# Kernel optimization log

Measured on AMD Instinct MI355X. Metric: run time of the kernel, lower is better.

The kernel has to match this reference:

```python
import jax, jax.numpy as jnp
import numpy as np

IMG_H, IMG_W = 16, 16
N = IMG_H * IMG_W              # 256 tokens
HEADS = 8
HEAD_DIM = 32
INNER = HEADS * HEAD_DIM       # 256
IN_CH = 256
OUT_CH = 256
BATCH = 64
SCALE = HEAD_DIM ** -0.5


def _make_relative_index():
    # Mirrors the torch buffer construction exactly.
    coords = np.stack(np.meshgrid(np.arange(IMG_H), np.arange(IMG_W), indexing='ij'))
    coords = coords.reshape(2, -1)                      # (2, N)
    rel = coords[:, :, None] - coords[:, None, :]       # (2, N, N)
    rel[0] += IMG_H - 1
    rel[1] += IMG_W - 1
    rel[0] *= 2 * IMG_W - 1
    idx = rel.sum(0).reshape(-1)                        # (N*N,) values in [0, (2H-1)(2W-1))
    return idx.astype(np.int32)


def setup_inputs() -> dict:
    key = jax.random.key(0)
    k1, k2, k3, k4, k5 = jax.random.split(key, 5)
    x = jax.random.normal(k1, (BATCH, N, IN_CH), dtype=jnp.float32)
    w_qkv = jax.random.normal(k2, (IN_CH, 3 * INNER), dtype=jnp.float32) * 0.02
    bias_table = jax.random.normal(k3, ((2 * IMG_H - 1) * (2 * IMG_W - 1), HEADS), dtype=jnp.float32) * 0.02
    w_out = jax.random.normal(k4, (INNER, OUT_CH), dtype=jnp.float32) * 0.02
    b_out = jax.random.normal(k5, (OUT_CH,), dtype=jnp.float32) * 0.02
    rel_index = jnp.asarray(_make_relative_index())
    return {"x": x, "w_qkv": w_qkv, "bias_table": bias_table,
            "w_out": w_out, "b_out": b_out, "rel_index": rel_index}


def reference(x, w_qkv, bias_table, w_out, b_out, rel_index):
    b, n, _ = x.shape
    qkv = x @ w_qkv                                     # (b, n, 3*inner)
    q, k, v = jnp.split(qkv, 3, axis=-1)
    def heads(t):
        return t.reshape(b, n, HEADS, HEAD_DIM).transpose(0, 2, 1, 3)  # (b, h, n, d)
    q, k, v = heads(q), heads(k), heads(v)
    dots = jnp.einsum('bhid,bhjd->bhij', q, k) * SCALE  # (b, h, n, n)
    # gather relative position bias: (n*n, h) -> (1, h, n, n)
    rel_bias = bias_table[rel_index].reshape(n, n, HEADS).transpose(2, 0, 1)[None]
    attn = jax.nn.softmax(dots + rel_bias, axis=-1)
    out = jnp.einsum('bhij,bhjd->bhid', attn, v)        # (b, h, n, d)
    out = out.transpose(0, 2, 1, 3).reshape(b, n, INNER)
    return out @ w_out + b_out
```

## Files before the change

kernel.cpp:

```cpp
#include <hip/hip_runtime.h>
#include <hip/hip_bf16.h>

typedef __bf16 bfv8 __attribute__((ext_vector_type(8)));
typedef float f32x4 __attribute__((ext_vector_type(4)));
typedef unsigned short u16;
typedef unsigned int u32;
typedef u16 u16x8 __attribute__((ext_vector_type(8)));

__device__ __forceinline__ float bf2f(u16 u){ union{u32 i; float f;} x; x.i=(u32)u<<16; return x.f; }
__device__ __forceinline__ u16 f2bf(float f){ union{float f; u32 i;} x; x.f=f; u32 i=x.i; return (u16)((i + 0x7FFFu + ((i>>16)&1u))>>16); }

__global__ __launch_bounds__(256) void transpose_k(const float* __restrict__ in, u16* __restrict__ out, int R, int C){
  __shared__ u16 tile[32][34];
  int c0 = blockIdx.x*32, r0 = blockIdx.y*32;
  int tx = threadIdx.x & 31, ty = threadIdx.x >> 5;
  #pragma unroll
  for(int dy=0; dy<32; dy+=8) tile[ty+dy][tx] = f2bf(in[(size_t)(r0+ty+dy)*C + (c0+tx)]);
  __syncthreads();
  #pragma unroll
  for(int dy=0; dy<32; dy+=8) out[(size_t)(c0+ty+dy)*R + (r0+tx)] = tile[tx][ty+dy];
}

__global__ __launch_bounds__(256) void biasgather_k(const float* __restrict__ bt, const int* __restrict__ ridx, u16* __restrict__ biasp2){
  const float L2E = 1.4426950408889634f;
  int idx = blockIdx.x*256 + threadIdx.x;
  int e = idx & 7, ch = (idx>>3)&7, lane = (idx>>6)&63, rb = (idx>>12)&15, h = (idx>>16)&7;
  int ll = lane & 15, lg = lane >> 4;
  int tj = ch*2 + (e>>2), r = e & 3;
  int q = rb*16 + ll, k = 16*tj + 4*lg + r;
  biasp2[idx] = f2bf(bt[ridx[q*256 + k]*8 + h] * L2E);
}

template<bool BIAS, typename OUT, bool AF32, int TM>
__global__ __launch_bounds__(256,4) void gemm_k(const void* __restrict__ Av, const u16* __restrict__ Bt,
                         const float* __restrict__ bias, OUT* __restrict__ C, int M, int N, int K){
  constexpr int MI = TM/32;
  __shared__ u16 As[TM][40];
  __shared__ u16 Bs[128][40];
  const int tid = threadIdx.x, lane = tid & 63, wv = tid >> 6;
  const int lg = lane >> 4, ll = lane & 15;
  const int wr = (wv >> 1)*(TM/2), wc = (wv & 1)*64;
  const size_t m0 = (size_t)blockIdx.x*TM;
  const int n0 = blockIdx.y*128;
  f32x4 acc[MI][4] = {};
  for(int k0=0; k0<K; k0+=32){
    #pragma unroll
    for(int p=0;p<TM/64;++p){
      int ch = tid + p*256;
      int row = ch >> 2, c8 = (ch & 3)*8;
      if constexpr (AF32){
        const float* Af = (const float*)Av;
        float4 a = *(const float4*)&Af[(m0+row)*(size_t)K + k0 + c8];
        float4 b = *(const float4*)&Af[(m0+row)*(size_t)K + k0 + c8 + 4];
        u16 r[8] = { f2bf(a.x),f2bf(a.y),f2bf(a.z),f2bf(a.w), f2bf(b.x),f2bf(b.y),f2bf(b.z),f2bf(b.w) };
        *(int4*)&As[row][c8] = *(int4*)r;
      } else {
        const u16* Ab = (const u16*)Av;
        *(int4*)&As[row][c8] = *(const int4*)&Ab[(m0+row)*(size_t)K + k0 + c8];
      }
    }
    #pragma unroll
    for(int p=0;p<2;++p){
      int ch = tid + p*256;
      int row = ch >> 2, c8 = (ch & 3)*8;
      *(int4*)&Bs[row][c8] = *(const int4*)&Bt[(size_t)(n0+row)*K + k0 + c8];
    }
    __syncthreads();
    bfv8 af[MI], bfr[4];
    #pragma unroll
    for(int i=0;i<MI;++i) af[i] = *(const bfv8*)&As[wr+16*i+ll][lg*8];
    #pragma unroll
    for(int j=0;j<4;++j) bfr[j] = *(const bfv8*)&Bs[wc+16*j+ll][lg*8];
    #pragma unroll
    for(int i=0;i<MI;++i)
      #pragma unroll
      for(int j=0;j<4;++j)
        acc[i][j] = __builtin_amdgcn_mfma_f32_16x16x32_bf16(af[i], bfr[j], acc[i][j], 0,0,0);
    __syncthreads();
  }
  #pragma unroll
  for(int i=0;i<MI;++i)
    #pragma unroll
    for(int j=0;j<4;++j){
      int col = n0 + wc + 16*j + ll;
      float bv = 0.f;
      if (BIAS) bv = bias[col];
      #pragma unroll
      for(int r=0;r<4;++r){
        size_t row = m0 + wr + 16*i + lg*4 + r;
        float v = acc[i][j][r] + bv;
        if constexpr (sizeof(OUT) == 2) C[row*(size_t)N + col] = f2bf(v);
        else                            C[row*(size_t)N + col] = v;
      }
    }
}

__global__ __launch_bounds__(256,3) void attn_k(const u16* __restrict__ qkv, const u16* __restrict__ biasp2, u16* __restrict__ attnb){
  __shared__ u16 Ks[256*40];
  __shared__ u16 Vt[32*264];
  const int bh = blockIdx.x >> 2, quarter = blockIdx.x & 3;
  const int b = bh >> 3, h = bh & 7;
  const int tid = threadIdx.x, lane = tid & 63, wv = tid >> 6;
  const int lg = lane >> 4, ll = lane & 15;
  const u16* qb = qkv + (size_t)b*256*768;
  const int q0 = quarter*64 + wv*16;
  const u16* bp = biasp2 + ((((size_t)h*16 + (q0>>4))*64 + lane) << 6);
  u16x8 bias[8];
  #pragma unroll
  for(int g=0; g<8; ++g) bias[g] = *(const u16x8*)&bp[g*8];
  bfv8 qf = *(const bfv8*)&qb[(size_t)(q0+ll)*768 + h*32 + lg*8];
  #pragma unroll
  for(int p=0;p<4;++p){
    int ch = tid + p*256;
    int j = ch >> 2, d8 = (ch & 3)*8;
    *(int4*)&Ks[j*40 + d8] = *(const int4*)&qb[(size_t)j*768 + 256 + h*32 + d8];
  }
  #pragma unroll
  for(int it=0; it<16; ++it){
    int e = tid + it*256;
    int j = e >> 4, dp = (e & 15)*2;
    int jp = ((j>>5)<<5) + 8*((j>>2)&3) + 4*((j>>4)&1) + (j&3);
    u32 v = *(const u32*)&qb[(size_t)j*768 + 512 + h*32 + dp];
    Vt[dp*264 + jp]     = (u16)(v & 0xffffu);
    Vt[(dp+1)*264 + jp] = (u16)(v >> 16);
  }
  __syncthreads();
  f32x4 s[16];
  const f32x4 zero = {0.f,0.f,0.f,0.f};
  #pragma unroll
  for(int tj=0;tj<16;++tj){
    bfv8 kf = *(const bfv8*)&Ks[(16*tj+ll)*40 + lg*8];
    s[tj] = __builtin_amdgcn_mfma_f32_16x16x32_bf16(kf, qf, zero, 0,0,0);
  }
  const float SCALE2 = 0.17677669529663687f * 1.4426950408889634f;
  f32x4 sm = {0.f,0.f,0.f,0.f};
  #pragma unroll
  for(int tj=0;tj<16;++tj){
    #pragma unroll
    for(int r=0;r<4;++r){
      float p = exp2f(fmaf(s[tj][r], SCALE2, bf2f(bias[tj>>1][4*(tj&1)+r])));
      s[tj][r] = p;
      sm[r] += p;
    }
  }
  float sum = sm[0]+sm[1]+sm[2]+sm[3];
  sum += __shfl_xor(sum,16);
  sum += __shfl_xor(sum,32);
  float rinv = 1.0f/sum;
  u32 pk[16][2];
  #pragma unroll
  for(int tj=0;tj<16;++tj){
    asm("v_cvt_pk_bf16_f32 %0, %1, %2" : "=v"(pk[tj][0]) : "v"(s[tj][0]), "v"(s[tj][1]));
    asm("v_cvt_pk_bf16_f32 %0, %1, %2" : "=v"(pk[tj][1]) : "v"(s[tj][2]), "v"(s[tj][3]));
  }
  f32x4 o[2] = {zero, zero};
  #pragma unroll
  for(int c=0;c<8;++c){
    union { u32 u[4]; bfv8 v; } pu;
    pu.u[0] = pk[2*c][0]; pu.u[1] = pk[2*c][1]; pu.u[2] = pk[2*c+1][0]; pu.u[3] = pk[2*c+1][1];
    bfv8 pf = pu.v;
    #pragma unroll
    for(int td=0;td<2;++td){
      bfv8 vf = *(const bfv8*)&Vt[(16*td+ll)*264 + 32*c + lg*8];
      o[td] = __builtin_amdgcn_mfma_f32_16x16x32_bf16(pf, vf, o[td], 0,0,0);
    }
  }
  #pragma unroll
  for(int td=0;td<2;++td)
    #pragma unroll
    for(int r=0;r<4;++r){
      float rl = __shfl(rinv, 4*lg + r);
      int row = q0 + 4*lg + r;
      attnb[((size_t)b*256 + row)*256 + h*32 + 16*td + ll] = f2bf(o[td][r]*rl);
    }
}

extern "C" void kernel_launch(void* const* d_in, const int* in_sizes, int n_in,
                              void* d_out, int out_size, void* d_ws, size_t ws_size,
                              hipStream_t stream) {
  const float* x     = (const float*)d_in[0];
  const float* w_qkv = (const float*)d_in[1];
  const float* btab  = (const float*)d_in[2];
  const float* w_out = (const float*)d_in[3];
  const float* b_out = (const float*)d_in[4];
  const int*   ridx  = (const int*)d_in[5];
  float* out = (float*)d_out;

  char* ws = (char*)d_ws;
  size_t off = 0;
  u16*   wT     = (u16*)(ws + off); off += (size_t)768*256*2;
  u16*   woT    = (u16*)(ws + off); off += (size_t)256*256*2;
  u16*   biasp2 = (u16*)(ws + off); off += (size_t)524288*2;
  u16*   qkvb   = (u16*)(ws + off); off += (size_t)64*256*768*2;
  u16*   attnb  = (u16*)(ws + off); off += (size_t)64*256*256*2;

  transpose_k<<<dim3(24,8),256,0,stream>>>(w_qkv, wT, 256, 768);
  transpose_k<<<dim3(8,8),256,0,stream>>>(w_out, woT, 256, 256);
  biasgather_k<<<2048,256,0,stream>>>(btab, ridx, biasp2);
  gemm_k<false,u16,true,128><<<dim3(128,6),256,0,stream>>>(x, wT, nullptr, qkvb, 16384, 768, 256);
  attn_k<<<2048,256,0,stream>>>(qkvb, biasp2, attnb);
  gemm_k<true,float,false,64><<<dim3(256,2),256,0,stream>>>(attnb, woT, b_out, out, 16384, 256, 256);
}
```

Measured before the change: 66.56 us.

## Merge prep kernels, pre-convert x, use direct LDS loads, loop attention quarters

Folds the two weight transposes and the bias gather into one prep kernel, which also converts x to bf16 up front. The GEMM now stages A and B tiles with global_load_lds straight into LDS using a K-step of 64. The attention kernel loads K/V once per (batch, head) and loops over the four query quarters instead of launching four blocks that each reload them. This cuts launch count and redundant K/V staging. The costs are an extra pass that writes and rereads a bf16 copy of x, a smaller attention grid (512 blocks), and unpadded LDS rows in the GEMM that may cause bank conflicts.

```diff
diff --git a/kernel.cpp b/kernel.cpp
--- a/kernel.cpp
+++ b/kernel.cpp
@@ -10,72 +10,94 @@
 __device__ __forceinline__ float bf2f(u16 u){ union{u32 i; float f;} x; x.i=(u32)u<<16; return x.f; }
 __device__ __forceinline__ u16 f2bf(float f){ union{float f; u32 i;} x; x.f=f; u32 i=x.i; return (u16)((i + 0x7FFFu + ((i>>16)&1u))>>16); }
 
-__global__ __launch_bounds__(256) void transpose_k(const float* __restrict__ in, u16* __restrict__ out, int R, int C){
+__device__ __forceinline__ void gl16(const void* g, void* l){
+  __builtin_amdgcn_global_load_lds((const __attribute__((address_space(1))) unsigned int*)g,
+                                   (__attribute__((address_space(3))) unsigned int*)l, 16, 0, 0);
+}
+
+__global__ __launch_bounds__(256) void prep_k(const float* __restrict__ x, u16* __restrict__ xb,
+                                              const float* __restrict__ w_qkv, u16* __restrict__ wT,
+                                              const float* __restrict__ w_out, u16* __restrict__ woT,
+                                              const float* __restrict__ bt, const int* __restrict__ ridx,
+                                              u16* __restrict__ biasp2){
   __shared__ u16 tile[32][34];
-  int c0 = blockIdx.x*32, r0 = blockIdx.y*32;
-  int tx = threadIdx.x & 31, ty = threadIdx.x >> 5;
-  #pragma unroll
-  for(int dy=0; dy<32; dy+=8) tile[ty+dy][tx] = f2bf(in[(size_t)(r0+ty+dy)*C + (c0+tx)]);
-  __syncthreads();
-  #pragma unroll
-  for(int dy=0; dy<32; dy+=8) out[(size_t)(c0+ty+dy)*R + (r0+tx)] = tile[tx][ty+dy];
-}
-
-__global__ __launch_bounds__(256) void biasgather_k(const float* __restrict__ bt, const int* __restrict__ ridx, u16* __restrict__ biasp2){
-  const float L2E = 1.4426950408889634f;
-  int idx = blockIdx.x*256 + threadIdx.x;
-  int e = idx & 7, ch = (idx>>3)&7, lane = (idx>>6)&63, rb = (idx>>12)&15, h = (idx>>16)&7;
-  int ll = lane & 15, lg = lane >> 4;
-  int tj = ch*2 + (e>>2), r = e & 3;
-  int q = rb*16 + ll, k = 16*tj + 4*lg + r;
-  biasp2[idx] = f2bf(bt[ridx[q*256 + k]*8 + h] * L2E);
-}
-
-template<bool BIAS, typename OUT, bool AF32, int TM>
-__global__ __launch_bounds__(256,4) void gemm_k(const void* __restrict__ Av, const u16* __restrict__ Bt,
+  const int bid = blockIdx.x, tid = threadIdx.x;
+  if (bid < 2048){
+    int i = (bid*256 + tid)*8;
+    float4 a = *(const float4*)&x[i];
+    float4 b = *(const float4*)&x[i+4];
+    u16 r[8] = { f2bf(a.x),f2bf(a.y),f2bf(a.z),f2bf(a.w), f2bf(b.x),f2bf(b.y),f2bf(b.z),f2bf(b.w) };
+    *(int4*)&xb[i] = *(int4*)r;
+  } else if (bid < 2048+192){
+    int b2 = bid - 2048;
+    int c0 = (b2 % 24)*32, r0 = (b2/24)*32;
+    int tx = tid & 31, ty = tid >> 5;
+    #pragma unroll
+    for(int dy=0; dy<32; dy+=8) tile[ty+dy][tx] = f2bf(w_qkv[(size_t)(r0+ty+dy)*768 + (c0+tx)]);
+    __syncthreads();
+    #pragma unroll
+    for(int dy=0; dy<32; dy+=8) wT[(size_t)(c0+ty+dy)*256 + (r0+tx)] = tile[tx][ty+dy];
+  } else if (bid < 2048+192+64){
+    int b3 = bid - (2048+192);
+    int c0 = (b3 & 7)*32, r0 = (b3 >> 3)*32;
+    int tx = tid & 31, ty = tid >> 5;
+    #pragma unroll
+    for(int dy=0; dy<32; dy+=8) tile[ty+dy][tx] = f2bf(w_out[(size_t)(r0+ty+dy)*256 + (c0+tx)]);
+    __syncthreads();
+    #pragma unroll
+    for(int dy=0; dy<32; dy+=8) woT[(size_t)(c0+ty+dy)*256 + (r0+tx)] = tile[tx][ty+dy];
+  } else {
+    const float L2E = 1.4426950408889634f;
+    int idx = (bid - (2048+192+64))*256 + tid;
+    int e = idx & 7, ch = (idx>>3)&7, lane = (idx>>6)&63, rb = (idx>>12)&15, h = (idx>>16)&7;
+    int ll = lane & 15, lg = lane >> 4;
+    int tj = ch*2 + (e>>2), r = e & 3;
+    int q = rb*16 + ll, k = 16*tj + 4*lg + r;
+    biasp2[idx] = f2bf(bt[ridx[q*256 + k]*8 + h] * L2E);
+  }
+}
+
+template<bool BIAS, typename OUT, int TM>
+__global__ __launch_bounds__(256) void gemm_k(const u16* __restrict__ A, const u16* __restrict__ Bt,
                          const float* __restrict__ bias, OUT* __restrict__ C, int M, int N, int K){
   constexpr int MI = TM/32;
-  __shared__ u16 As[TM][40];
-  __shared__ u16 Bs[128][40];
+  __shared__ u16 As[TM*64];
+  __shared__ u16 Bs[128*64];
   const int tid = threadIdx.x, lane = tid & 63, wv = tid >> 6;
   const int lg = lane >> 4, ll = lane & 15;
   const int wr = (wv >> 1)*(TM/2), wc = (wv & 1)*64;
   const size_t m0 = (size_t)blockIdx.x*TM;
   const int n0 = blockIdx.y*128;
+  const int lrow = lane >> 3, lcol = (lane & 7)*8;
   f32x4 acc[MI][4] = {};
-  for(int k0=0; k0<K; k0+=32){
-    #pragma unroll
-    for(int p=0;p<TM/64;++p){
-      int ch = tid + p*256;
-      int row = ch >> 2, c8 = (ch & 3)*8;
-      if constexpr (AF32){
-        const float* Af = (const float*)Av;
-        float4 a = *(const float4*)&Af[(m0+row)*(size_t)K + k0 + c8];
-        float4 b = *(const float4*)&Af[(m0+row)*(size_t)K + k0 + c8 + 4];
-        u16 r[8] = { f2bf(a.x),f2bf(a.y),f2bf(a.z),f2bf(a.w), f2bf(b.x),f2bf(b.y),f2bf(b.z),f2bf(b.w) };
-        *(int4*)&As[row][c8] = *(int4*)r;
-      } else {
-        const u16* Ab = (const u16*)Av;
-        *(int4*)&As[row][c8] = *(const int4*)&Ab[(m0+row)*(size_t)K + k0 + c8];
-      }
-    }
-    #pragma unroll
-    for(int p=0;p<2;++p){
-      int ch = tid + p*256;
-      int row = ch >> 2, c8 = (ch & 3)*8;
-      *(int4*)&Bs[row][c8] = *(const int4*)&Bt[(size_t)(n0+row)*K + k0 + c8];
-    }
-    __syncthreads();
-    bfv8 af[MI], bfr[4];
-    #pragma unroll
-    for(int i=0;i<MI;++i) af[i] = *(const bfv8*)&As[wr+16*i+ll][lg*8];
-    #pragma unroll
-    for(int j=0;j<4;++j) bfr[j] = *(const bfv8*)&Bs[wc+16*j+ll][lg*8];
+  for(int k0=0; k0<K; k0+=64){
+    #pragma unroll
+    for(int c=0;c<MI;++c){
+      int rowbase = (wv*MI + c)*8;
+      gl16(&A[(m0 + rowbase + lrow)*(size_t)K + k0 + lcol], &As[rowbase*64]);
+    }
+    #pragma unroll
+    for(int c=0;c<4;++c){
+      int rowbase = (wv*4 + c)*8;
+      gl16(&Bt[(size_t)(n0 + rowbase + lrow)*K + k0 + lcol], &Bs[rowbase*64]);
+    }
+    __syncthreads();
+    bfv8 af[MI][2], bf[4][2];
     #pragma unroll
     for(int i=0;i<MI;++i)
       #pragma unroll
-      for(int j=0;j<4;++j)
-        acc[i][j] = __builtin_amdgcn_mfma_f32_16x16x32_bf16(af[i], bfr[j], acc[i][j], 0,0,0);
+      for(int kh=0;kh<2;++kh) af[i][kh] = *(const bfv8*)&As[(wr+16*i+ll)*64 + kh*32 + lg*8];
+    #pragma unroll
+    for(int j=0;j<4;++j)
+      #pragma unroll
+      for(int kh=0;kh<2;++kh) bf[j][kh] = *(const bfv8*)&Bs[(wc+16*j+ll)*64 + kh*32 + lg*8];
+    #pragma unroll
+    for(int kh=0;kh<2;++kh)
+      #pragma unroll
+      for(int i=0;i<MI;++i)
+        #pragma unroll
+        for(int j=0;j<4;++j)
+          acc[i][j] = __builtin_amdgcn_mfma_f32_16x16x32_bf16(af[i][kh], bf[j][kh], acc[i][j], 0,0,0);
     __syncthreads();
   }
   #pragma unroll
@@ -98,17 +120,10 @@
 __global__ __launch_bounds__(256,3) void attn_k(const u16* __restrict__ qkv, const u16* __restrict__ biasp2, u16* __restrict__ attnb){
   __shared__ u16 Ks[256*40];
   __shared__ u16 Vt[32*264];
-  const int bh = blockIdx.x >> 2, quarter = blockIdx.x & 3;
-  const int b = bh >> 3, h = bh & 7;
+  const int b = blockIdx.x >> 3, h = blockIdx.x & 7;
   const int tid = threadIdx.x, lane = tid & 63, wv = tid >> 6;
   const int lg = lane >> 4, ll = lane & 15;
   const u16* qb = qkv + (size_t)b*256*768;
-  const int q0 = quarter*64 + wv*16;
-  const u16* bp = biasp2 + ((((size_t)h*16 + (q0>>4))*64 + lane) << 6);
-  u16x8 bias[8];
-  #pragma unroll
-  for(int g=0; g<8; ++g) bias[g] = *(const u16x8*)&bp[g*8];
-  bfv8 qf = *(const bfv8*)&qb[(size_t)(q0+ll)*768 + h*32 + lg*8];
   #pragma unroll
   for(int p=0;p<4;++p){
     int ch = tid + p*256;
@@ -125,54 +140,63 @@
     Vt[(dp+1)*264 + jp] = (u16)(v >> 16);
   }
   __syncthreads();
-  f32x4 s[16];
+  const float SCALE2 = 0.17677669529663687f * 1.4426950408889634f;
   const f32x4 zero = {0.f,0.f,0.f,0.f};
-  #pragma unroll
-  for(int tj=0;tj<16;++tj){
-    bfv8 kf = *(const bfv8*)&Ks[(16*tj+ll)*40 + lg*8];
-    s[tj] = __builtin_amdgcn_mfma_f32_16x16x32_bf16(kf, qf, zero, 0,0,0);
-  }
-  const float SCALE2 = 0.17677669529663687f * 1.4426950408889634f;
-  f32x4 sm = {0.f,0.f,0.f,0.f};
-  #pragma unroll
-  for(int tj=0;tj<16;++tj){
-    #pragma unroll
-    for(int r=0;r<4;++r){
-      float p = exp2f(fmaf(s[tj][r], SCALE2, bf2f(bias[tj>>1][4*(tj&1)+r])));
-      s[tj][r] = p;
-      sm[r] += p;
-    }
-  }
-  float sum = sm[0]+sm[1]+sm[2]+sm[3];
-  sum += __shfl_xor(sum,16);
-  sum += __shfl_xor(sum,32);
-  float rinv = 1.0f/sum;
-  u32 pk[16][2];
-  #pragma unroll
-  for(int tj=0;tj<16;++tj){
-    asm("v_cvt_pk_bf16_f32 %0, %1, %2" : "=v"(pk[tj][0]) : "v"(s[tj][0]), "v"(s[tj][1]));
-    asm("v_cvt_pk_bf16_f32 %0, %1, %2" : "=v"(pk[tj][1]) : "v"(s[tj][2]), "v"(s[tj][3]));
-  }
-  f32x4 o[2] = {zero, zero};
-  #pragma unroll
-  for(int c=0;c<8;++c){
-    union { u32 u[4]; bfv8 v; } pu;
-    pu.u[0] = pk[2*c][0]; pu.u[1] = pk[2*c][1]; pu.u[2] = pk[2*c+1][0]; pu.u[3] = pk[2*c+1][1];
-    bfv8 pf = pu.v;
-    #pragma unroll
-    for(int td=0;td<2;++td){
-      bfv8 vf = *(const bfv8*)&Vt[(16*td+ll)*264 + 32*c + lg*8];
-      o[td] = __builtin_amdgcn_mfma_f32_16x16x32_bf16(pf, vf, o[td], 0,0,0);
-    }
-  }
-  #pragma unroll
-  for(int td=0;td<2;++td)
-    #pragma unroll
-    for(int r=0;r<4;++r){
-      float rl = __shfl(rinv, 4*lg + r);
-      int row = q0 + 4*lg + r;
-      attnb[((size_t)b*256 + row)*256 + h*32 + 16*td + ll] = f2bf(o[td][r]*rl);
-    }
+  #pragma unroll 1
+  for(int quarter=0; quarter<4; ++quarter){
+    const int q0 = quarter*64 + wv*16;
+    const u16* bp = biasp2 + ((((size_t)h*16 + (q0>>4))*64 + lane) << 6);
+    u16x8 bias[8];
+    #pragma unroll
+    for(int g=0; g<8; ++g) bias[g] = *(const u16x8*)&bp[g*8];
+    bfv8 qf = *(const bfv8*)&qb[(size_t)(q0+ll)*768 + h*32 + lg*8];
+    f32x4 s[16];
+    #pragma unroll
+    for(int tj=0;tj<16;++tj){
+      bfv8 kf = *(const bfv8*)&Ks[(16*tj+ll)*40 + lg*8];
+      s[tj] = __builtin_amdgcn_mfma_f32_16x16x32_bf16(kf, qf, zero, 0,0,0);
+    }
+    f32x4 sm = {0.f,0.f,0.f,0.f};
+    #pragma unroll
+    for(int tj=0;tj<16;++tj){
+      #pragma unroll
+      for(int r=0;r<4;++r){
+        float p = exp2f(fmaf(s[tj][r], SCALE2, bf2f(bias[tj>>1][4*(tj&1)+r])));
+        s[tj][r] = p;
+        sm[r] += p;
+      }
+    }
+    float sum = sm[0]+sm[1]+sm[2]+sm[3];
+    sum += __shfl_xor(sum,16);
+    sum += __shfl_xor(sum,32);
+    float rinv = 1.0f/sum;
+    u32 pk[16][2];
+    #pragma unroll
+    for(int tj=0;tj<16;++tj){
+      asm("v_cvt_pk_bf16_f32 %0, %1, %2" : "=v"(pk[tj][0]) : "v"(s[tj][0]), "v"(s[tj][1]));
+      asm("v_cvt_pk_bf16_f32 %0, %1, %2" : "=v"(pk[tj][1]) : "v"(s[tj][2]), "v"(s[tj][3]));
+    }
+    f32x4 o[2] = {zero, zero};
+    #pragma unroll
+    for(int c=0;c<8;++c){
+      union { u32 u[4]; bfv8 v; } pu;
+      pu.u[0] = pk[2*c][0]; pu.u[1] = pk[2*c][1]; pu.u[2] = pk[2*c+1][0]; pu.u[3] = pk[2*c+1][1];
+      bfv8 pf = pu.v;
+      #pragma unroll
+      for(int td=0;td<2;++td){
+        bfv8 vf = *(const bfv8*)&Vt[(16*td+ll)*264 + 32*c + lg*8];
+        o[td] = __builtin_amdgcn_mfma_f32_16x16x32_bf16(pf, vf, o[td], 0,0,0);
+      }
+    }
+    #pragma unroll
+    for(int td=0;td<2;++td)
+      #pragma unroll
+      for(int r=0;r<4;++r){
+        float rl = __shfl(rinv, 4*lg + r);
+        int row = q0 + 4*lg + r;
+        attnb[((size_t)b*256 + row)*256 + h*32 + 16*td + ll] = f2bf(o[td][r]*rl);
+      }
+  }
 }
 
 extern "C" void kernel_launch(void* const* d_in, const int* in_sizes, int n_in,
@@ -188,16 +212,15 @@
 
   char* ws = (char*)d_ws;
   size_t off = 0;
+  u16*   xb     = (u16*)(ws + off); off += (size_t)64*256*256*2;
   u16*   wT     = (u16*)(ws + off); off += (size_t)768*256*2;
   u16*   woT    = (u16*)(ws + off); off += (size_t)256*256*2;
   u16*   biasp2 = (u16*)(ws + off); off += (size_t)524288*2;
   u16*   qkvb   = (u16*)(ws + off); off += (size_t)64*256*768*2;
   u16*   attnb  = (u16*)(ws + off); off += (size_t)64*256*256*2;
 
-  transpose_k<<<dim3(24,8),256,0,stream>>>(w_qkv, wT, 256, 768);
-  transpose_k<<<dim3(8,8),256,0,stream>>>(w_out, woT, 256, 256);
-  biasgather_k<<<2048,256,0,stream>>>(btab, ridx, biasp2);
-  gemm_k<false,u16,true,128><<<dim3(128,6),256,0,stream>>>(x, wT, nullptr, qkvb, 16384, 768, 256);
-  attn_k<<<2048,256,0,stream>>>(qkvb, biasp2, attnb);
-  gemm_k<true,float,false,64><<<dim3(256,2),256,0,stream>>>(attnb, woT, b_out, out, 16384, 256, 256);
-}
+  prep_k<<<2048+192+64+2048,256,0,stream>>>(x, xb, w_qkv, wT, w_out, woT, btab, ridx, biasp2);
+  gemm_k<false,u16,128><<<dim3(128,6),256,0,stream>>>(xb, wT, nullptr, qkvb, 16384, 768, 256);
+  attn_k<<<512,256,0,stream>>>(qkvb, biasp2, attnb);
+  gemm_k<true,float,64><<<dim3(256,2),256,0,stream>>>(attnb, woT, b_out, out, 16384, 256, 256);
+}
```

Result: faster. 62.78 us (-5.7%).
